# Performance work log

Hardware: AMD Instinct MI355X
Metric: run time of the kernel (lower is better)

The kernel has to match this reference:

```python
import jax, jax.numpy as jnp
import numpy as np
import math

FACTOR = 5


def setup_inputs() -> dict:
    key = jax.random.key(0)
    k1, k2, k3, k4 = jax.random.split(key, 4)
    B, L, H, D = 4, 2048, 8, 64
    sample_k = FACTOR * int(np.ceil(np.log(L)))  # 40
    queries = jax.random.normal(k1, (B, L, H, D), dtype=jnp.float32)
    keys = jax.random.normal(k2, (B, L, H, D), dtype=jnp.float32)
    values = jax.random.normal(k3, (B, L, H, D), dtype=jnp.float32)
    # per-query sampled key indices (replaces the host-side random.sample loop)
    index_sample = jax.random.randint(k4, (L, sample_k), 0, L, dtype=jnp.int64)
    return {"queries": queries, "keys": keys, "values": values,
            "index_sample": index_sample}


def reference(queries, keys, values, index_sample):
    B, L_Q, H, D = queries.shape
    L_K = keys.shape[1]
    # [B, L, H, D] -> [B, H, L, D]
    Q = jnp.transpose(queries, (0, 2, 1, 3))
    K = jnp.transpose(keys, (0, 2, 1, 3))
    V = jnp.transpose(values, (0, 2, 1, 3))

    u = min(FACTOR * int(np.ceil(np.log(L_Q))), L_Q)  # n_top

    # --- _prob_QK: sample-score-topk-gather ---
    # K_sample[b,h,i,s,e] = K[b,h,index_sample[i,s],e]  -> [B,H,L_Q,S,E]
    K_sample = K[:, :, index_sample, :]
    Q_K_sample = jnp.einsum('bhie,bhise->bhis', Q, K_sample)  # [B,H,L_Q,S]
    M = Q_K_sample.max(axis=-1) - Q_K_sample.sum(axis=-1) / L_K  # [B,H,L_Q]
    _, M_top = jax.lax.top_k(M, u)  # [B,H,u] indices of sparse queries

    Q_reduce = jnp.take_along_axis(Q, M_top[..., None], axis=2)  # [B,H,u,D]
    scores = jnp.einsum('bhue,bhke->bhuk', Q_reduce, K)  # [B,H,u,L_K]

    scale = 1.0 / math.sqrt(D)
    scores = scores * scale

    # --- initial context (mask_flag=True): causal running sum of V ---
    context = jnp.cumsum(V, axis=2)  # [B,H,L_Q,D]

    # --- ProbMask: causal mask rows gathered at M_top ---
    causal_mask = jnp.arange(L_K)[None, None, None, :] > M_top[..., None]
    scores = jnp.where(causal_mask, -jnp.inf, scores)
    attn = jax.nn.softmax(scores, axis=-1)  # [B,H,u,L_K]

    update = jnp.einsum('bhuk,bhkd->bhud', attn, V)  # [B,H,u,D]
    bi = jnp.arange(B)[:, None, None]
    hi = jnp.arange(H)[None, :, None]
    context = context.at[bi, hi, M_top].set(update)

    # back to [B, L, H, D]
    return jnp.transpose(context, (0, 2, 1, 3))
```

## Files before the change

kernel.cpp:

```cpp
#include <hip/hip_runtime.h>
#include <hip/hip_bf16.h>
#include <math.h>


#define BB 4
#define LL 2048
#define HH 8
#define DD 64
#define SS 40
#define UU 40
#define CC 64
#define LC (LL/CC)

#define KC    64
#define NCH2  8
#define UG    2
#define KSUB  4
#define KPAD  68
#define PPAD  68

__global__ void k_measure(const float* __restrict__ Q, const float* __restrict__ K,
                          const int* __restrict__ idx, float* __restrict__ M)
{
    __shared__ float sMax[4][8];
    __shared__ float sSum[4][8];

    int t   = threadIdx.x;
    int blk = blockIdx.x;
    int b   = blk >> 11;
    int i   = blk & (LL - 1);
    int w    = t >> 6, lane = t & 63;
    int hg   = lane >> 4;
    int d4   = lane & 15;

    const int*   ip   = idx + (size_t)i * SS + w * 10;
    const float* Kb   = K + (size_t)b * (LL * HH * DD);
    const float* Qrow = Q + ((size_t)b * LL + i) * (HH * DD);

    float4 qa = *(const float4*)(Qrow + hg * DD + d4 * 4);
    float4 qb = *(const float4*)(Qrow + (4 + hg) * DD + d4 * 4);

    float maxa = -INFINITY, suma = 0.f;
    float maxb = -INFINITY, sumb = 0.f;

#define DOT4(q_, k_) (fmaf((q_).w, (k_).w, fmaf((q_).z, (k_).z, \
                      fmaf((q_).y, (k_).y, (q_).x * (k_).x))))
    #pragma unroll
    for (int u = 0; u < 10; u += 2) {
        int k0 = ip[u], k1 = ip[u + 1];
        const float* r0 = Kb + (size_t)k0 * (HH * DD);
        const float* r1 = Kb + (size_t)k1 * (HH * DD);
        float4 a0 = *(const float4*)(r0 + hg * DD + d4 * 4);
        float4 b0 = *(const float4*)(r0 + (4 + hg) * DD + d4 * 4);
        float4 a1 = *(const float4*)(r1 + hg * DD + d4 * 4);
        float4 b1 = *(const float4*)(r1 + (4 + hg) * DD + d4 * 4);

        float pa0 = DOT4(qa, a0), pb0 = DOT4(qb, b0);
        float pa1 = DOT4(qa, a1), pb1 = DOT4(qb, b1);

        #pragma unroll
        for (int off = 1; off < 16; off <<= 1) {
            pa0 += __shfl_xor(pa0, off);
            pb0 += __shfl_xor(pb0, off);
            pa1 += __shfl_xor(pa1, off);
            pb1 += __shfl_xor(pb1, off);
        }
        maxa = fmaxf(maxa, fmaxf(pa0, pa1));  suma += pa0 + pa1;
        maxb = fmaxf(maxb, fmaxf(pb0, pb1));  sumb += pb0 + pb1;
    }
#undef DOT4

    if (d4 == 0) {
        sMax[w][hg]     = maxa;  sSum[w][hg]     = suma;
        sMax[w][4 + hg] = maxb;  sSum[w][4 + hg] = sumb;
    }
    __syncthreads();

    if (t < 8) {
        float mx = sMax[0][t], sm = sSum[0][t];
        #pragma unroll
        for (int w2 = 1; w2 < 4; ++w2) {
            mx = fmaxf(mx, sMax[w2][t]);
            sm += sSum[w2][t];
        }
        M[((size_t)(b * HH + t)) * LL + i] = mx - sm * (1.0f / (float)LL);
    }
}

__global__ void k_topk(const float* __restrict__ M, int* __restrict__ topIdx)
{
    int lane = threadIdx.x;
    int bh   = blockIdx.x;
    const float* Mp = M + (size_t)bh * LL;

    unsigned k[32];
    #pragma unroll
    for (int r = 0; r < 32; ++r) {
        unsigned u = __float_as_uint(Mp[r * 64 + lane]);
        k[r] = (u & 0x80000000u) ? ~u : (u | 0x80000000u);
    }

    unsigned T = 0u;
    for (int bit = 31; bit >= 0; --bit) {
        unsigned cand = T | (1u << bit);
        int c = 0;
        #pragma unroll
        for (int r = 0; r < 32; ++r) c += (k[r] >= cand) ? 1 : 0;
        #pragma unroll
        for (int off = 1; off < 64; off <<= 1) c += __shfl_xor(c, off);
        if (c >= UU) T = cand;
    }

    int cGT = 0, cGE = 0;
    #pragma unroll
    for (int r = 0; r < 32; ++r) {
        cGT += (k[r] > T) ? 1 : 0;
        cGE += (k[r] >= T) ? 1 : 0;
    }
    #pragma unroll
    for (int off = 1; off < 64; off <<= 1) {
        cGT += __shfl_xor(cGT, off);
        cGE += __shfl_xor(cGE, off);
    }

    int need = UU - cGT;
    int X = LL;
    if (cGE - cGT != need) {
        int lo2 = 0;
        for (int bit = 10; bit >= 0; --bit) {
            int cand = lo2 | (1 << bit);
            int c = 0;
            #pragma unroll
            for (int r = 0; r < 32; ++r)
                c += (k[r] == T && (r * 64 + lane) < cand) ? 1 : 0;
            #pragma unroll
            for (int off = 1; off < 64; off <<= 1) c += __shfl_xor(c, off);
            if (c < need) lo2 = cand;
        }
        X = lo2 + 1;
    }

    unsigned inMask = 0u;
    int cnt = 0;
    #pragma unroll
    for (int r = 0; r < 32; ++r) {
        bool in = (k[r] > T) || (k[r] == T && (r * 64 + lane) < X);
        if (in) { inMask |= 1u << r; ++cnt; }
    }
    int pre = cnt;
    #pragma unroll
    for (int off = 1; off < 64; off <<= 1) {
        int v = __shfl_up(pre, off);
        if (lane >= off) pre += v;
    }
    int slot = pre - cnt;
    #pragma unroll
    for (int r = 0; r < 32; ++r) {
        if ((inMask >> r) & 1u) {
            topIdx[bh * UU + slot] = r * 64 + lane;
            ++slot;
        }
    }
}

__launch_bounds__(256, 2)
__global__ void k_attn(const float* __restrict__ Q, const float* __restrict__ K,
                       const float* __restrict__ V, const int* __restrict__ topIdx,
                       float* __restrict__ Oc, float* __restrict__ Lc)
{
    __shared__ float sK[2][KC][KPAD];
    __shared__ float sV[2][KC][KPAD];
    __shared__ float sP[20][PPAD];
    __shared__ int   sPos[UU];

    int t   = threadIdx.x;
    int bid = blockIdx.x;
    int bh  = bid / (NCH2 * UG);
    int rem = bid % (NCH2 * UG);
    int ch  = rem / UG, ug = rem % UG;
    int b   = bh / HH, h = bh % HH;

    if (t < UU) sPos[t] = topIdx[bh * UU + t];

    int j  = t & 63;
    int w  = t >> 6, lane = t & 63;
    int ub = __builtin_amdgcn_readfirstlane(w) * 5;

    int d4p = t & 15, tg = t >> 4;
    float4 a0 = {0,0,0,0}, a1 = {0,0,0,0};
    float den[5] = {0.f, 0.f, 0.f, 0.f, 0.f};

    const float* Kh = K + ((size_t)b * LL * HH + h) * DD;
    const float* Vh = V + ((size_t)b * LL * HH + h) * DD;

    float4 pk0, pk1, pk2, pk3, pv0, pv1, pv2, pv3;

#define ISSUE(k0_) { \
    size_t g0 = (size_t)((k0_) +  0 + tg) * (HH * DD) + d4p * 4; \
    size_t g1 = (size_t)((k0_) + 16 + tg) * (HH * DD) + d4p * 4; \
    size_t g2 = (size_t)((k0_) + 32 + tg) * (HH * DD) + d4p * 4; \
    size_t g3 = (size_t)((k0_) + 48 + tg) * (HH * DD) + d4p * 4; \
    pk0 = *(const float4*)(Kh + g0); pv0 = *(const float4*)(Vh + g0); \
    pk1 = *(const float4*)(Kh + g1); pv1 = *(const float4*)(Vh + g1); \
    pk2 = *(const float4*)(Kh + g2); pv2 = *(const float4*)(Vh + g2); \
    pk3 = *(const float4*)(Kh + g3); pv3 = *(const float4*)(Vh + g3); \
}
#define COMMIT(buf_) { \
    *(float4*)&sK[buf_][ 0 + tg][d4p * 4] = pk0; *(float4*)&sV[buf_][ 0 + tg][d4p * 4] = pv0; \
    *(float4*)&sK[buf_][16 + tg][d4p * 4] = pk1; *(float4*)&sV[buf_][16 + tg][d4p * 4] = pv1; \
    *(float4*)&sK[buf_][32 + tg][d4p * 4] = pk2; *(float4*)&sV[buf_][32 + tg][d4p * 4] = pv2; \
    *(float4*)&sK[buf_][48 + tg][d4p * 4] = pk3; *(float4*)&sV[buf_][48 + tg][d4p * 4] = pv3; \
}

    int k0base = ch * KSUB * KC;
    ISSUE(k0base);
    COMMIT(0);
    __syncthreads();

    #pragma unroll
    for (int sub = 0; sub < KSUB; ++sub) {
        int cur = sub & 1;
        int k0  = k0base + sub * KC;

        if (sub + 1 < KSUB) ISSUE(k0 + KC);

        int jg = k0 + j;
        {
            int p0 = __builtin_amdgcn_readfirstlane(sPos[ug * 20 + ub + 0]);
            int p1 = __builtin_amdgcn_readfirstlane(sPos[ug * 20 + ub + 1]);
            int p2 = __builtin_amdgcn_readfirstlane(sPos[ug * 20 + ub + 2]);
            int p3 = __builtin_amdgcn_readfirstlane(sPos[ug * 20 + ub + 3]);
            int p4 = __builtin_amdgcn_readfirstlane(sPos[ug * 20 + ub + 4]);
            const float* q0 = Q + (((size_t)b * LL + p0) * HH + h) * DD;
            const float* q1 = Q + (((size_t)b * LL + p1) * HH + h) * DD;
            const float* q2 = Q + (((size_t)b * LL + p2) * HH + h) * DD;
            const float* q3 = Q + (((size_t)b * LL + p3) * HH + h) * DD;
            const float* q4 = Q + (((size_t)b * LL + p4) * HH + h) * DD;
            float c0 = 0.f, c1 = 0.f, c2 = 0.f, c3 = 0.f, c4 = 0.f;
            #pragma unroll
            for (int d4 = 0; d4 < 16; ++d4) {
                float4 kk = *(const float4*)&sK[cur][j][d4 * 4];
                int d = d4 * 4;
                c0 = fmaf(kk.x, q0[d], c0); c0 = fmaf(kk.y, q0[d+1], c0);
                c0 = fmaf(kk.z, q0[d+2], c0); c0 = fmaf(kk.w, q0[d+3], c0);
                c1 = fmaf(kk.x, q1[d], c1); c1 = fmaf(kk.y, q1[d+1], c1);
                c1 = fmaf(kk.z, q1[d+2], c1); c1 = fmaf(kk.w, q1[d+3], c1);
                c2 = fmaf(kk.x, q2[d], c2); c2 = fmaf(kk.y, q2[d+1], c2);
                c2 = fmaf(kk.z, q2[d+2], c2); c2 = fmaf(kk.w, q2[d+3], c2);
                c3 = fmaf(kk.x, q3[d], c3); c3 = fmaf(kk.y, q3[d+1], c3);
                c3 = fmaf(kk.z, q3[d+2], c3); c3 = fmaf(kk.w, q3[d+3], c3);
                c4 = fmaf(kk.x, q4[d], c4); c4 = fmaf(kk.y, q4[d+1], c4);
                c4 = fmaf(kk.z, q4[d+2], c4); c4 = fmaf(kk.w, q4[d+3], c4);
            }
            float e0 = (jg > p0) ? 0.f : __expf(c0 * 0.125f);
            float e1 = (jg > p1) ? 0.f : __expf(c1 * 0.125f);
            float e2 = (jg > p2) ? 0.f : __expf(c2 * 0.125f);
            float e3 = (jg > p3) ? 0.f : __expf(c3 * 0.125f);
            float e4 = (jg > p4) ? 0.f : __expf(c4 * 0.125f);
            sP[ub + 0][j] = e0;
            sP[ub + 1][j] = e1;
            sP[ub + 2][j] = e2;
            sP[ub + 3][j] = e3;
            sP[ub + 4][j] = e4;
            #pragma unroll
            for (int off = 1; off < 64; off <<= 1) {
                e0 += __shfl_xor(e0, off);
                e1 += __shfl_xor(e1, off);
                e2 += __shfl_xor(e2, off);
                e3 += __shfl_xor(e3, off);
                e4 += __shfl_xor(e4, off);
            }
            den[0] += e0; den[1] += e1; den[2] += e2; den[3] += e3; den[4] += e4;
        }
        __syncthreads();

        if (sub + 1 < KSUB) {
            if (cur == 0) { COMMIT(1); } else { COMMIT(0); }
        }

        #pragma unroll 4
        for (int j4 = 0; j4 < KC / 4; ++j4) {
            float4 pj0 = *(const float4*)&sP[tg][j4 * 4];
            float4 pj1 = (tg < 4) ? *(const float4*)&sP[16 + tg][j4 * 4]
                                  : (float4){0,0,0,0};
            float4 va = *(const float4*)&sV[cur][j4 * 4 + 0][d4p * 4];
            float4 vb = *(const float4*)&sV[cur][j4 * 4 + 1][d4p * 4];
            float4 vc = *(const float4*)&sV[cur][j4 * 4 + 2][d4p * 4];
            float4 vd = *(const float4*)&sV[cur][j4 * 4 + 3][d4p * 4];
            a0.x = fmaf(pj0.x, va.x, fmaf(pj0.y, vb.x, fmaf(pj0.z, vc.x, fmaf(pj0.w, vd.x, a0.x))));
            a0.y = fmaf(pj0.x, va.y, fmaf(pj0.y, vb.y, fmaf(pj0.z, vc.y, fmaf(pj0.w, vd.y, a0.y))));
            a0.z = fmaf(pj0.x, va.z, fmaf(pj0.y, vb.z, fmaf(pj0.z, vc.z, fmaf(pj0.w, vd.z, a0.z))));
            a0.w = fmaf(pj0.x, va.w, fmaf(pj0.y, vb.w, fmaf(pj0.z, vc.w, fmaf(pj0.w, vd.w, a0.w))));
            a1.x = fmaf(pj1.x, va.x, fmaf(pj1.y, vb.x, fmaf(pj1.z, vc.x, fmaf(pj1.w, vd.x, a1.x))));
            a1.y = fmaf(pj1.x, va.y, fmaf(pj1.y, vb.y, fmaf(pj1.z, vc.y, fmaf(pj1.w, vd.y, a1.y))));
            a1.z = fmaf(pj1.x, va.z, fmaf(pj1.y, vb.z, fmaf(pj1.z, vc.z, fmaf(pj1.w, vd.z, a1.z))));
            a1.w = fmaf(pj1.x, va.w, fmaf(pj1.y, vb.w, fmaf(pj1.z, vc.w, fmaf(pj1.w, vd.w, a1.w))));
        }
        __syncthreads();
    }
#undef ISSUE
#undef COMMIT

    if (lane == 0) {
        int base = (bh * NCH2 + ch) * UU + ug * 20 + ub;
        Lc[base + 0] = den[0]; Lc[base + 1] = den[1]; Lc[base + 2] = den[2];
        Lc[base + 3] = den[3]; Lc[base + 4] = den[4];
    }
    {
        int u0g = ug * 20 + tg;
        size_t o0 = ((size_t)(bh * NCH2 + ch) * UU + u0g) * DD + d4p * 4;
        *(float4*)(Oc + o0) = a0;
        if (tg < 4) {
            int u1g = ug * 20 + 16 + tg;
            size_t o1 = ((size_t)(bh * NCH2 + ch) * UU + u1g) * DD + d4p * 4;
            *(float4*)(Oc + o1) = a1;
        }
    }
}

__global__ void k_chunksum(const float* __restrict__ V, float* __restrict__ chunkSum)
{
    int t  = threadIdx.x;
    int c  = blockIdx.x % CC;
    int bh = blockIdx.x / CC;
    int b  = bh / HH; int h = bh - b * HH;
    int d4 = t & 15, rs = t >> 4;

    float4 acc = {0,0,0,0};
    int l0 = c * LC;
    for (int l = l0 + rs; l < l0 + LC; l += 4) {
        float4 v = *(const float4*)(V + (((size_t)b * LL + l) * HH + h) * DD + d4 * 4);
        acc.x += v.x; acc.y += v.y; acc.z += v.z; acc.w += v.w;
    }
    acc.x += __shfl_xor(acc.x, 16); acc.y += __shfl_xor(acc.y, 16);
    acc.z += __shfl_xor(acc.z, 16); acc.w += __shfl_xor(acc.w, 16);
    acc.x += __shfl_xor(acc.x, 32); acc.y += __shfl_xor(acc.y, 32);
    acc.z += __shfl_xor(acc.z, 32); acc.w += __shfl_xor(acc.w, 32);
    if (t < 16)
        *(float4*)(chunkSum + ((size_t)bh * CC + c) * DD + d4 * 4) = acc;
}

__global__ void k_cumsum(const float* __restrict__ V, const float* __restrict__ chunkSum,
                         float* __restrict__ out)
{
    int t  = threadIdx.x;
    int c  = blockIdx.x & (CC - 1);
    int bh = blockIdx.x >> 6;
    int b  = bh / HH; int h = bh - b * HH;
    int d4 = t & 15, s = t >> 4;

    const float4* CS4 = (const float4*)chunkSum;
    float4 off = {0,0,0,0};
    for (int c2 = s; c2 < c; c2 += 4) {
        float4 x = CS4[((size_t)bh * CC + c2) * 16 + d4];
        off.x += x.x; off.y += x.y; off.z += x.z; off.w += x.w;
    }
    off.x += __shfl_xor(off.x, 16); off.y += __shfl_xor(off.y, 16);
    off.z += __shfl_xor(off.z, 16); off.w += __shfl_xor(off.w, 16);
    off.x += __shfl_xor(off.x, 32); off.y += __shfl_xor(off.y, 32);
    off.z += __shfl_xor(off.z, 32); off.w += __shfl_xor(off.w, 32);

    int l0 = c * LC + s * 8;
    size_t base = (((size_t)b * LL + l0) * HH + h) * DD + d4 * 4;
    const size_t stride = (size_t)HH * DD;

    float4 v[8];
    #pragma unroll
    for (int r = 0; r < 8; ++r)
        v[r] = *(const float4*)(V + base + (size_t)r * stride);
    #pragma unroll
    for (int r = 1; r < 8; ++r) {
        v[r].x += v[r-1].x; v[r].y += v[r-1].y;
        v[r].z += v[r-1].z; v[r].w += v[r-1].w;
    }

    float4 inc = v[7];
    float4 p1;
    p1.x = __shfl_up(inc.x, 16); p1.y = __shfl_up(inc.y, 16);
    p1.z = __shfl_up(inc.z, 16); p1.w = __shfl_up(inc.w, 16);
    if (s >= 1) { inc.x += p1.x; inc.y += p1.y; inc.z += p1.z; inc.w += p1.w; }
    float4 p2;
    p2.x = __shfl_up(inc.x, 32); p2.y = __shfl_up(inc.y, 32);
    p2.z = __shfl_up(inc.z, 32); p2.w = __shfl_up(inc.w, 32);
    if (s >= 2) { inc.x += p2.x; inc.y += p2.y; inc.z += p2.z; inc.w += p2.w; }

    float4 add;
    add.x = off.x + inc.x - v[7].x;
    add.y = off.y + inc.y - v[7].y;
    add.z = off.z + inc.z - v[7].z;
    add.w = off.w + inc.w - v[7].w;

    #pragma unroll
    for (int r = 0; r < 8; ++r) {
        float4 o;
        o.x = v[r].x + add.x; o.y = v[r].y + add.y;
        o.z = v[r].z + add.z; o.w = v[r].w + add.w;
        *(float4*)(out + base + (size_t)r * stride) = o;
    }
}

__global__ void k_finalize(const float* __restrict__ Oc, const float* __restrict__ Lc,
                           const int* __restrict__ topIdx, float* __restrict__ out)
{
    int bh = blockIdx.x;
    int b  = bh / HH, h = bh % HH;
    int t  = threadIdx.x;
    int d  = t & 63, w = t >> 6;
    for (int i = 0; i < 10; ++i) {
        int u = w * 10 + i;
        int pos = topIdx[bh * UU + u];
        float num = 0.f, den = 0.f;
        #pragma unroll
        for (int c = 0; c < NCH2; ++c) {
            num += Oc[((size_t)(bh * NCH2 + c) * UU + u) * DD + d];
            den += Lc[(bh * NCH2 + c) * UU + u];
        }
        out[(((size_t)b * LL + pos) * HH + h) * DD + d] = num / den;
    }
}

extern "C" void kernel_launch(void* const* d_in, const int* in_sizes, int n_in,
                              void* d_out, int out_size, void* d_ws, size_t ws_size,
                              hipStream_t stream)
{
    const float* Q   = (const float*)d_in[0];
    const float* K   = (const float*)d_in[1];
    const float* V   = (const float*)d_in[2];
    const int*   idx = (const int*)d_in[3];
    float* out = (float*)d_out;

    float* M        = (float*)d_ws;
    int*   topIdx   = (int*)(M + (size_t)BB * HH * LL);
    float* Oc       = (float*)(topIdx + BB * HH * UU);
    float* Lc       = Oc + (size_t)BB * HH * NCH2 * UU * DD;
    float* chunkSum = Lc + BB * HH * NCH2 * UU;

    k_measure <<<BB * LL,             256, 0, stream>>>(Q, K, idx, M);
    k_topk    <<<BB * HH,              64, 0, stream>>>(M, topIdx);
    k_attn    <<<BB * HH * NCH2 * UG, 256, 0, stream>>>(Q, K, V, topIdx, Oc, Lc);
    k_chunksum<<<BB * HH * CC,         64, 0, stream>>>(V, chunkSum);
    k_cumsum  <<<BB * HH * CC,         64, 0, stream>>>(V, chunkSum, out);
    k_finalize<<<BB * HH,             256, 0, stream>>>(Oc, Lc, topIdx, out);
}
```

Before: 186.7 us.

## Software-pipeline sampled K loads and fuse finalize into cumsum kernel

The measure kernel now double-buffers the gathered K rows, issuing the next pair's loads before computing the current pair's dot products, with a sched_barrier to keep that order. This is meant to hide gather latency. The separate finalize kernel is removed. Each cumsum block checks whether any top-k position falls in its chunk and, if so, overwrites those rows with the normalized attention output after waiting for its own stores. This saves one kernel launch but adds a 40-entry topIdx scan to every cumsum block. It also relies on the per-block store ordering for the overwrite to be correct.

```diff
diff --git a/kernel.cpp b/kernel.cpp
--- a/kernel.cpp
+++ b/kernel.cpp
@@ -45,19 +45,34 @@
 
 #define DOT4(q_, k_) (fmaf((q_).w, (k_).w, fmaf((q_).z, (k_).z, \
                       fmaf((q_).y, (k_).y, (q_).x * (k_).x))))
-    #pragma unroll
-    for (int u = 0; u < 10; u += 2) {
-        int k0 = ip[u], k1 = ip[u + 1];
+
+    float4 A0, B0, A1, B1;
+    float4 A2, B2, A3, B3;
+    {
+        int k0 = ip[0], k1 = ip[1];
         const float* r0 = Kb + (size_t)k0 * (HH * DD);
         const float* r1 = Kb + (size_t)k1 * (HH * DD);
-        float4 a0 = *(const float4*)(r0 + hg * DD + d4 * 4);
-        float4 b0 = *(const float4*)(r0 + (4 + hg) * DD + d4 * 4);
-        float4 a1 = *(const float4*)(r1 + hg * DD + d4 * 4);
-        float4 b1 = *(const float4*)(r1 + (4 + hg) * DD + d4 * 4);
-
-        float pa0 = DOT4(qa, a0), pb0 = DOT4(qb, b0);
-        float pa1 = DOT4(qa, a1), pb1 = DOT4(qb, b1);
-
+        A0 = *(const float4*)(r0 + hg * DD + d4 * 4);
+        B0 = *(const float4*)(r0 + (4 + hg) * DD + d4 * 4);
+        A1 = *(const float4*)(r1 + hg * DD + d4 * 4);
+        B1 = *(const float4*)(r1 + (4 + hg) * DD + d4 * 4);
+    }
+
+    #pragma unroll
+    for (int g = 0; g < 5; ++g) {
+        if (g < 4) {
+            int k2 = ip[2 * g + 2], k3 = ip[2 * g + 3];
+            const float* r2 = Kb + (size_t)k2 * (HH * DD);
+            const float* r3 = Kb + (size_t)k3 * (HH * DD);
+            A2 = *(const float4*)(r2 + hg * DD + d4 * 4);
+            B2 = *(const float4*)(r2 + (4 + hg) * DD + d4 * 4);
+            A3 = *(const float4*)(r3 + hg * DD + d4 * 4);
+            B3 = *(const float4*)(r3 + (4 + hg) * DD + d4 * 4);
+        }
+        __builtin_amdgcn_sched_barrier(0);
+
+        float pa0 = DOT4(qa, A0), pb0 = DOT4(qb, B0);
+        float pa1 = DOT4(qa, A1), pb1 = DOT4(qb, B1);
         #pragma unroll
         for (int off = 1; off < 16; off <<= 1) {
             pa0 += __shfl_xor(pa0, off);
@@ -67,6 +82,8 @@
         }
         maxa = fmaxf(maxa, fmaxf(pa0, pa1));  suma += pa0 + pa1;
         maxb = fmaxf(maxb, fmaxf(pb0, pb1));  sumb += pb0 + pb1;
+
+        A0 = A2; B0 = B2; A1 = A3; B1 = B3;
     }
 #undef DOT4
 
@@ -341,7 +358,8 @@
 }
 
 __global__ void k_cumsum(const float* __restrict__ V, const float* __restrict__ chunkSum,
-                         float* __restrict__ out)
+                         const float* __restrict__ Oc, const float* __restrict__ Lc,
+                         const int* __restrict__ topIdx, float* __restrict__ out)
 {
     int t  = threadIdx.x;
     int c  = blockIdx.x & (CC - 1);
@@ -397,25 +415,28 @@
         o.z = v[r].z + add.z; o.w = v[r].w + add.w;
         *(float4*)(out + base + (size_t)r * stride) = o;
     }
-}
-
-__global__ void k_finalize(const float* __restrict__ Oc, const float* __restrict__ Lc,
-                           const int* __restrict__ topIdx, float* __restrict__ out)
-{
-    int bh = blockIdx.x;
-    int b  = bh / HH, h = bh % HH;
-    int t  = threadIdx.x;
-    int d  = t & 63, w = t >> 6;
-    for (int i = 0; i < 10; ++i) {
-        int u = w * 10 + i;
+
+    int l0c = c * LC;
+    int anyTop = 0;
+    #pragma unroll
+    for (int u = 0; u < UU; ++u) {
         int pos = topIdx[bh * UU + u];
-        float num = 0.f, den = 0.f;
-        #pragma unroll
-        for (int c = 0; c < NCH2; ++c) {
-            num += Oc[((size_t)(bh * NCH2 + c) * UU + u) * DD + d];
-            den += Lc[(bh * NCH2 + c) * UU + u];
-        }
-        out[(((size_t)b * LL + pos) * HH + h) * DD + d] = num / den;
+        anyTop |= (pos >= l0c && pos < l0c + LC) ? 1 : 0;
+    }
+    if (anyTop) {
+        asm volatile("s_waitcnt vmcnt(0)" ::: "memory");
+        for (int u = 0; u < UU; ++u) {
+            int pos = topIdx[bh * UU + u];
+            if (pos >= l0c && pos < l0c + LC) {
+                float num = 0.f, den = 0.f;
+                #pragma unroll
+                for (int cc = 0; cc < NCH2; ++cc) {
+                    num += Oc[((size_t)(bh * NCH2 + cc) * UU + u) * DD + t];
+                    den += Lc[(bh * NCH2 + cc) * UU + u];
+                }
+                out[(((size_t)b * LL + pos) * HH + h) * DD + t] = num / den;
+            }
+        }
     }
 }
 
@@ -439,6 +460,5 @@
     k_topk    <<<BB * HH,              64, 0, stream>>>(M, topIdx);
     k_attn    <<<BB * HH * NCH2 * UG, 256, 0, stream>>>(Q, K, V, topIdx, Oc, Lc);
     k_chunksum<<<BB * HH * CC,         64, 0, stream>>>(V, chunkSum);
-    k_cumsum  <<<BB * HH * CC,         64, 0, stream>>>(V, chunkSum, out);
-    k_finalize<<<BB * HH,             256, 0, stream>>>(Oc, Lc, topIdx, out);
-}
+    k_cumsum  <<<BB * HH * CC,         64, 0, stream>>>(V, chunkSum, Oc, Lc, topIdx, out);
+}
```

After: 185.5 us. About the same (-0.6%).
